# Kernel tuning notes

Hardware: AMD Instinct MI355X
Metric: run time of the kernel (lower is better)

## Reference

```python
import jax, jax.numpy as jnp
import numpy as np

UNITS = 512


def setup_inputs() -> dict:
    key = jax.random.key(0)
    ks = jax.random.split(key, 9)
    B, D, U = 16384, 512, UNITS
    return {
        "inputs": jax.random.normal(ks[0], (B, 2 * D), dtype=jnp.float32),
        "h": jax.random.normal(ks[1], (B, U), dtype=jnp.float32),
        "w_z": jax.random.normal(ks[2], (D, U), dtype=jnp.float32) * 0.05,
        "u_z": jax.random.normal(ks[3], (U, U), dtype=jnp.float32) * 0.05,
        "b_z": jnp.zeros((U,), dtype=jnp.float32),
        "w_r": jax.random.normal(ks[4], (D, U), dtype=jnp.float32) * 0.05,
        "u_r": jax.random.normal(ks[5], (U, U), dtype=jnp.float32) * 0.05,
        "b_r": jnp.zeros((U,), dtype=jnp.float32),
        "w_h": jax.random.normal(ks[6], (D, U), dtype=jnp.float32) * 0.05,
        "u_h": jax.random.normal(ks[7], (U, U), dtype=jnp.float32) * 0.05,
        "b_h": jnp.zeros((U,), dtype=jnp.float32),
    }


def reference(inputs, h, w_z, u_z, b_z, w_r, u_r, b_r, w_h, u_h, b_h):
    # Split concatenated (input, mask) halves along the feature axis.
    x, mask = jnp.split(inputs, 2, axis=1)  # each (B, D)
    # Faithful to source: mask @ zeros((D, U)) is identically zero.
    out_mask = jnp.matmul(mask, jnp.zeros((mask.shape[-1], UNITS), dtype=inputs.dtype))  # (B, U)
    h_masked = h * out_mask
    z_t = jax.nn.sigmoid(jnp.matmul(x, w_z) + jnp.matmul(h_masked, u_z) + b_z)
    r_t = jax.nn.sigmoid(jnp.matmul(x, w_r) + jnp.matmul(h_masked, u_r) + b_r)
    h_t = jnp.tanh(jnp.matmul(x, w_h) + jnp.matmul(r_t * h_masked, u_h) + b_h)
    h_t_seq = z_t * h_t + (1.0 - z_t) * h_masked  # (B, U)
    h_t_forward = jnp.concatenate((h_t_seq, out_mask), axis=1)  # (B, 2U)
    return (h_t_forward, h_t_seq)
```

## Files before the change

### kernel.cpp

```cpp
#include <hip/hip_runtime.h>

typedef __attribute__((ext_vector_type(4))) float f32x4;
typedef __attribute__((ext_vector_type(8))) short short8;
typedef __attribute__((ext_vector_type(8))) unsigned short ushort8;
typedef __attribute__((ext_vector_type(4))) unsigned short ushort4v;

#define M_ROWS 16384
#define KDIM 512
#define UDIM 512
#define IN_STRIDE 1024
#define NSTEP 16

__device__ __forceinline__ unsigned short f2bf(float f) {
    union { float f; unsigned u; } v; v.f = f;
    unsigned r = v.u + 0x7FFFu + ((v.u >> 16) & 1u);
    return (unsigned short)(r >> 16);
}

#define GLD16(g, l)                                                            \
    __builtin_amdgcn_global_load_lds(                                          \
        (const __attribute__((address_space(1))) void*)(g),                    \
        (__attribute__((address_space(3))) void*)(l), 16, 0, 0)

__global__ __launch_bounds__(256) void pack_all(
    const float* __restrict__ inp,
    const float* __restrict__ w_z,
    const float* __restrict__ w_h,
    unsigned short* __restrict__ Ap,
    unsigned short* __restrict__ Wp)
{
    const int bid = blockIdx.x;
    if (bid < 256) {
        int tid = bid * 256 + threadIdx.x;
        int s   = tid & 511;
        int kt  = (tid >> 9) & 15;
        int ub  = tid >> 13;
        int jj  = s >> 2;
        int sl  = (s & 3) ^ ((jj >> 1) & 3);
        int k   = kt * 32 + sl * 8;
        const float* w = ((jj >> 5) & 1) ? w_h : w_z;
        int u = ub * 64 + ((jj >> 6) << 5) + (jj & 31);
        ushort8 v;
#pragma unroll
        for (int i = 0; i < 8; ++i)
            v[i] = f2bf(w[(size_t)(k + i) * UDIM + u]);
        *reinterpret_cast<ushort8*>(Wp + (size_t)tid * 8) = v;
    } else {
        int g   = (bid - 256) * 256 + threadIdx.x;
        int by  = g >> 13;
        int rem = g & 8191;
        int kt  = rem >> 9;
        int s   = rem & 511;
        int row = by * 128 + (s >> 2);
        int sl  = (s & 3) ^ ((s >> 3) & 3);
        int k   = kt * 32 + sl * 8;
        const float* p = inp + (size_t)row * IN_STRIDE + k;
        f32x4 a = *reinterpret_cast<const f32x4*>(p);
        f32x4 b = *reinterpret_cast<const f32x4*>(p + 4);
        ushort8 v;
        v[0] = f2bf(a[0]); v[1] = f2bf(a[1]); v[2] = f2bf(a[2]); v[3] = f2bf(a[3]);
        v[4] = f2bf(b[0]); v[5] = f2bf(b[1]); v[6] = f2bf(b[2]); v[7] = f2bf(b[3]);
        *reinterpret_cast<ushort8*>(Ap + (size_t)g * 8) = v;
    }
}

__global__ __launch_bounds__(256, 3) void gru_gemm(
    const unsigned short* __restrict__ Ap,
    const unsigned short* __restrict__ Wp,
    const float* __restrict__ b_z,
    const float* __restrict__ b_h,
    float* __restrict__ out)
{
    __shared__ __align__(16) unsigned char smem[49152];
    unsigned short* shA = (unsigned short*)smem;
    unsigned short* shB = (unsigned short*)(smem + 24576);

    const int tid  = threadIdx.x;
    const int lane = tid & 63;
    const int wid  = tid >> 6;
    const int wm   = wid >> 1;
    const int wn   = wid & 1;

    const int d  = blockIdx.x;
    const int bx = (d >> 3) & 7;
    const int by = (d & 7) * 16 + (d >> 6);
    const int u0   = bx * 64;
    const int brow = by * 128;

    const int s0 = wid * 128 + lane;
    const unsigned short* ap = Ap + (size_t)by * 65536 + (size_t)s0 * 8;
    const unsigned short* bp = Wp + (size_t)bx * 65536 + (size_t)s0 * 8;

    f32x4 acc[4][4];
#pragma unroll
    for (int m = 0; m < 4; ++m)
#pragma unroll
        for (int n = 0; n < 4; ++n)
            acc[m][n] = (f32x4){0.f, 0.f, 0.f, 0.f};

    auto STAGE = [&](int b, int t) {
        GLD16(ap + t * 4096,       shA + b * 4096 + wid * 1024);
        GLD16(ap + t * 4096 + 512, shA + b * 4096 + wid * 1024 + 512);
        GLD16(bp + t * 4096,       shB + b * 4096 + wid * 1024);
        GLD16(bp + t * 4096 + 512, shB + b * 4096 + wid * 1024 + 512);
    };

    const int fr = lane & 15;
    const int ks = lane >> 4;
    const int xo = (fr >> 1) & 3;
    int aoff[4], boff[4];
#pragma unroll
    for (int m = 0; m < 4; ++m)
        aoff[m] = (wm * 64 + m * 16 + fr) * 32 + ((ks ^ xo) << 3);
#pragma unroll
    for (int n = 0; n < 4; ++n)
        boff[n] = (wn * 64 + n * 16 + fr) * 32 + ((ks ^ xo) << 3);

    STAGE(0, 0);
    STAGE(1, 1);
    asm volatile("s_waitcnt vmcnt(4)" ::: "memory");
    asm volatile("s_barrier" ::: "memory");

#pragma unroll
    for (int t = 0; t < NSTEP; ++t) {
        if (t + 2 < NSTEP) STAGE((t + 2) % 3, t + 2);
        const int buf = t % 3;
        short8 af[4], bfrag[4];
#pragma unroll
        for (int m = 0; m < 4; ++m)
            af[m] = *reinterpret_cast<const short8*>(&shA[buf * 4096 + aoff[m]]);
#pragma unroll
        for (int n = 0; n < 4; ++n)
            bfrag[n] = *reinterpret_cast<const short8*>(&shB[buf * 4096 + boff[n]]);
#pragma unroll
        for (int m = 0; m < 4; ++m)
#pragma unroll
            for (int n = 0; n < 4; ++n)
                acc[m][n] = __builtin_amdgcn_mfma_f32_16x16x32_bf16(af[m], bfrag[n], acc[m][n], 0, 0, 0);
        if (t + 1 < NSTEP) {
            asm volatile("s_waitcnt lgkmcnt(0)" ::: "memory");
            if (t + 2 < NSTEP) {
                asm volatile("s_waitcnt vmcnt(4)" ::: "memory");
            } else {
                asm volatile("s_waitcnt vmcnt(0)" ::: "memory");
            }
            asm volatile("s_barrier" ::: "memory");
        }
    }

    __syncthreads();

    float* plane = (float*)smem;
    const int fq = lane >> 4;
#pragma unroll
    for (int p = 0; p < 2; ++p) {
        int ucol = wn * 32 + p * 16 + fr;
        float bz = b_z[u0 + ucol];
        float bh = b_h[u0 + ucol];
#pragma unroll
        for (int m = 0; m < 4; ++m) {
            int row0 = wm * 64 + m * 16 + fq * 4;
            f32x4 az = acc[m][p];
            f32x4 ah = acc[m][p + 2];
#pragma unroll
            for (int j = 0; j < 4; ++j) {
                float zt = 1.f / (1.f + __expf(-(az[j] + bz)));
                float e  = __expf(2.f * (ah[j] + bh));
                float s  = zt * (1.f - 2.f / (e + 1.f));
                plane[(row0 + j) * 68 + ucol] = s;
            }
        }
    }
    __syncthreads();

    float* fwd = out;
    float* seq = out + (size_t)M_ROWS * 1024;
    const f32x4 z4 = (f32x4){0.f, 0.f, 0.f, 0.f};
    const int c4 = (tid & 15) * 4;
#pragma unroll
    for (int it = 0; it < 8; ++it) {
        int row = it * 16 + (tid >> 4);
        f32x4 v = *reinterpret_cast<const f32x4*>(&plane[row * 68 + c4]);
        size_t grow = (size_t)(brow + row);
        *reinterpret_cast<f32x4*>(&fwd[grow * 1024 + u0 + c4])       = v;
        *reinterpret_cast<f32x4*>(&fwd[grow * 1024 + 512 + u0 + c4]) = z4;
        *reinterpret_cast<f32x4*>(&seq[grow * 512 + u0 + c4])        = v;
    }
}

#define LDSS 40
__global__ __launch_bounds__(256) void gru_fused_legacy(
    const float* __restrict__ inp, const float* __restrict__ w_z,
    const float* __restrict__ b_z, const float* __restrict__ w_h,
    const float* __restrict__ b_h, float* __restrict__ out)
{
    __shared__ __align__(16) unsigned short Asl[2][128][LDSS];
    __shared__ __align__(16) unsigned short Bsl[2][128][LDSS];
    const int tid = threadIdx.x, lane = tid & 63, wid = tid >> 6;
    const int wm = wid >> 1, wn = wid & 1;
    const int u0 = blockIdx.x * 64, brow = blockIdx.y * 128;
    f32x4 acc[4][4];
#pragma unroll
    for (int m = 0; m < 4; ++m)
#pragma unroll
        for (int n = 0; n < 4; ++n) acc[m][n] = (f32x4){0.f,0.f,0.f,0.f};
    f32x4 rA[4], rB[4];
#define STAGE_LOAD(kt) { const int k0_=(kt)*32; \
    _Pragma("unroll") for (int it=0; it<4; ++it){ int idx=tid+256*it; int r=idx>>3,c=(idx&7)<<2; \
        rA[it]=*reinterpret_cast<const f32x4*>(inp+(size_t)(brow+r)*IN_STRIDE+k0_+c);} \
    _Pragma("unroll") for (int it=0; it<4; ++it){ int idx=tid+256*it; int jj=idx&127; int k4=(idx>>7)<<2; \
        const float* w_=((jj>>5)&1)?w_h:w_z; int u_=u0+((jj>>6)<<5)+(jj&31); \
        const float* p_=w_+(size_t)(k0_+k4)*UDIM+u_; \
        rB[it][0]=p_[0]; rB[it][1]=p_[UDIM]; rB[it][2]=p_[2*UDIM]; rB[it][3]=p_[3*UDIM];} }
#define STAGE_WRITE(bufi) { \
    _Pragma("unroll") for (int it=0; it<4; ++it){ int idx=tid+256*it; int r=idx>>3,c=(idx&7)<<2; ushort4v v; \
        v[0]=f2bf(rA[it][0]); v[1]=f2bf(rA[it][1]); v[2]=f2bf(rA[it][2]); v[3]=f2bf(rA[it][3]); \
        *reinterpret_cast<ushort4v*>(&Asl[bufi][r][c])=v;} \
    _Pragma("unroll") for (int it=0; it<4; ++it){ int idx=tid+256*it; int jj=idx&127; int k4=(idx>>7)<<2; ushort4v v; \
        v[0]=f2bf(rB[it][0]); v[1]=f2bf(rB[it][1]); v[2]=f2bf(rB[it][2]); v[3]=f2bf(rB[it][3]); \
        *reinterpret_cast<ushort4v*>(&Bsl[bufi][jj][k4])=v;} }
    STAGE_LOAD(0); STAGE_WRITE(0);
    const int fr = lane & 15, koff = (lane >> 4) << 3;
    for (int kt = 0; kt < NSTEP; ++kt) {
        if (kt + 1 < NSTEP) STAGE_LOAD(kt + 1);
        __syncthreads();
        const int buf = kt & 1;
        short8 af[4], bfr[4];
#pragma unroll
        for (int m = 0; m < 4; ++m) af[m] = *reinterpret_cast<const short8*>(&Asl[buf][wm*64+m*16+fr][koff]);
#pragma unroll
        for (int n = 0; n < 4; ++n) bfr[n] = *reinterpret_cast<const short8*>(&Bsl[buf][wn*64+n*16+fr][koff]);
#pragma unroll
        for (int m = 0; m < 4; ++m)
#pragma unroll
            for (int n = 0; n < 4; ++n)
                acc[m][n] = __builtin_amdgcn_mfma_f32_16x16x32_bf16(af[m], bfr[n], acc[m][n], 0, 0, 0);
        if (kt + 1 < NSTEP) STAGE_WRITE((kt + 1) & 1);
    }
    float* fwd = out; float* seq = out + (size_t)M_ROWS * 1024;
    const int fq = lane >> 4;
#pragma unroll
    for (int p = 0; p < 2; ++p) {
        int u = u0 + wn * 32 + p * 16 + fr;
        float bz = b_z[u], bh = b_h[u];
#pragma unroll
        for (int m = 0; m < 4; ++m) {
            int row0 = brow + wm * 64 + m * 16 + fq * 4;
            f32x4 az = acc[m][p], ah = acc[m][p + 2];
#pragma unroll
            for (int j = 0; j < 4; ++j) {
                float zt = 1.f / (1.f + __expf(-(az[j] + bz)));
                float e  = __expf(2.f * (ah[j] + bh));
                float s  = zt * (1.f - 2.f / (e + 1.f));
                size_t rr = (size_t)(row0 + j);
                fwd[rr * 1024 + u] = s;
                fwd[rr * 1024 + 512 + u] = 0.f;
                seq[rr * 512 + u] = s;
            }
        }
    }
}

extern "C" void kernel_launch(void* const* d_in, const int* in_sizes, int n_in,
                              void* d_out, int out_size, void* d_ws, size_t ws_size,
                              hipStream_t stream) {
    const float* inp = (const float*)d_in[0];
    const float* w_z = (const float*)d_in[2];
    const float* b_z = (const float*)d_in[4];
    const float* w_h = (const float*)d_in[8];
    const float* b_h = (const float*)d_in[10];
    float* out = (float*)d_out;

    const size_t needA = (size_t)M_ROWS * KDIM * 2;
    const size_t needB = (size_t)8 * 16 * 512 * 16;
    if (ws_size >= needA + needB) {
        unsigned short* Ap = (unsigned short*)d_ws;
        unsigned short* Wp = (unsigned short*)((char*)d_ws + needA);
        hipLaunchKernelGGL(pack_all, dim3(256 + 4096), dim3(256), 0, stream,
                           inp, w_z, w_h, Ap, Wp);
        hipLaunchKernelGGL(gru_gemm, dim3(1024), dim3(256), 0, stream,
                           Ap, Wp, b_z, b_h, out);
    } else {
        hipLaunchKernelGGL(gru_fused_legacy, dim3(8, 128), dim3(256), 0, stream,
                           inp, w_z, b_z, w_h, b_h, out);
    }
}
```

Measured before the change: 46.54 us.

## Fuse activation fp32-to-bf16 conversion into GEMM prologue, drop A pack pass

Removes the separate packing pass that converted the x half of the inputs to swizzled bf16 in workspace. The GEMM now loads fp32 x directly into registers, converts to bf16 and writes swizzled tiles into a double-buffered LDS region, while B keeps the async global-to-LDS triple buffer. This cuts the extra global write and read of the packed A matrix and one kernel launch. In exchange it adds register pressure, conversion ALU work inside the main loop, and a synchronous LDS-write step before each barrier. Each A tile is also read as fp32 by all 8 column blocks.

```diff
diff --git a/kernel.cpp b/kernel.cpp
--- a/kernel.cpp
+++ b/kernel.cpp
@@ -22,58 +22,37 @@
         (const __attribute__((address_space(1))) void*)(g),                    \
         (__attribute__((address_space(3))) void*)(l), 16, 0, 0)
 
-__global__ __launch_bounds__(256) void pack_all(
-    const float* __restrict__ inp,
+__global__ __launch_bounds__(256) void pack_w(
     const float* __restrict__ w_z,
     const float* __restrict__ w_h,
-    unsigned short* __restrict__ Ap,
     unsigned short* __restrict__ Wp)
 {
-    const int bid = blockIdx.x;
-    if (bid < 256) {
-        int tid = bid * 256 + threadIdx.x;
-        int s   = tid & 511;
-        int kt  = (tid >> 9) & 15;
-        int ub  = tid >> 13;
-        int jj  = s >> 2;
-        int sl  = (s & 3) ^ ((jj >> 1) & 3);
-        int k   = kt * 32 + sl * 8;
-        const float* w = ((jj >> 5) & 1) ? w_h : w_z;
-        int u = ub * 64 + ((jj >> 6) << 5) + (jj & 31);
-        ushort8 v;
-#pragma unroll
-        for (int i = 0; i < 8; ++i)
-            v[i] = f2bf(w[(size_t)(k + i) * UDIM + u]);
-        *reinterpret_cast<ushort8*>(Wp + (size_t)tid * 8) = v;
-    } else {
-        int g   = (bid - 256) * 256 + threadIdx.x;
-        int by  = g >> 13;
-        int rem = g & 8191;
-        int kt  = rem >> 9;
-        int s   = rem & 511;
-        int row = by * 128 + (s >> 2);
-        int sl  = (s & 3) ^ ((s >> 3) & 3);
-        int k   = kt * 32 + sl * 8;
-        const float* p = inp + (size_t)row * IN_STRIDE + k;
-        f32x4 a = *reinterpret_cast<const f32x4*>(p);
-        f32x4 b = *reinterpret_cast<const f32x4*>(p + 4);
-        ushort8 v;
-        v[0] = f2bf(a[0]); v[1] = f2bf(a[1]); v[2] = f2bf(a[2]); v[3] = f2bf(a[3]);
-        v[4] = f2bf(b[0]); v[5] = f2bf(b[1]); v[6] = f2bf(b[2]); v[7] = f2bf(b[3]);
-        *reinterpret_cast<ushort8*>(Ap + (size_t)g * 8) = v;
-    }
+    int tid = blockIdx.x * 256 + threadIdx.x;
+    int s   = tid & 511;
+    int kt  = (tid >> 9) & 15;
+    int ub  = tid >> 13;
+    int jj  = s >> 2;
+    int sl  = (s & 3) ^ ((jj >> 1) & 3);
+    int k   = kt * 32 + sl * 8;
+    const float* w = ((jj >> 5) & 1) ? w_h : w_z;
+    int u = ub * 64 + ((jj >> 6) << 5) + (jj & 31);
+    ushort8 v;
+#pragma unroll
+    for (int i = 0; i < 8; ++i)
+        v[i] = f2bf(w[(size_t)(k + i) * UDIM + u]);
+    *reinterpret_cast<ushort8*>(Wp + (size_t)tid * 8) = v;
 }
 
 __global__ __launch_bounds__(256, 3) void gru_gemm(
-    const unsigned short* __restrict__ Ap,
+    const float* __restrict__ x,
     const unsigned short* __restrict__ Wp,
     const float* __restrict__ b_z,
     const float* __restrict__ b_h,
     float* __restrict__ out)
 {
-    __shared__ __align__(16) unsigned char smem[49152];
+    __shared__ __align__(16) unsigned char smem[40960];
     unsigned short* shA = (unsigned short*)smem;
-    unsigned short* shB = (unsigned short*)(smem + 24576);
+    unsigned short* shB = (unsigned short*)(smem + 16384);
 
     const int tid  = threadIdx.x;
     const int lane = tid & 63;
@@ -87,9 +66,15 @@
     const int u0   = bx * 64;
     const int brow = by * 128;
 
-    const int s0 = wid * 128 + lane;
-    const unsigned short* ap = Ap + (size_t)by * 65536 + (size_t)s0 * 8;
-    const unsigned short* bp = Wp + (size_t)bx * 65536 + (size_t)s0 * 8;
+    const int s0a = wid * 128 + lane;
+    const int s1a = s0a + 64;
+    const int r0 = s0a >> 2, r1 = s1a >> 2;
+    const int sl0 = (s0a & 3) ^ ((r0 >> 1) & 3);
+    const int sl1 = (s1a & 3) ^ ((r1 >> 1) & 3);
+    const float* g0 = x + (size_t)(brow + r0) * IN_STRIDE + sl0 * 8;
+    const float* g1 = x + (size_t)(brow + r1) * IN_STRIDE + sl1 * 8;
+
+    const unsigned short* bp = Wp + (size_t)bx * 65536 + (size_t)s0a * 8;
 
     f32x4 acc[4][4];
 #pragma unroll
@@ -98,12 +83,32 @@
         for (int n = 0; n < 4; ++n)
             acc[m][n] = (f32x4){0.f, 0.f, 0.f, 0.f};
 
-    auto STAGE = [&](int b, int t) {
-        GLD16(ap + t * 4096,       shA + b * 4096 + wid * 1024);
-        GLD16(ap + t * 4096 + 512, shA + b * 4096 + wid * 1024 + 512);
-        GLD16(bp + t * 4096,       shB + b * 4096 + wid * 1024);
-        GLD16(bp + t * 4096 + 512, shB + b * 4096 + wid * 1024 + 512);
-    };
+    f32x4 rA[2][4];
+
+#define ISSUE_A(t, set)                                                        \
+    {                                                                          \
+        rA[set][0] = *reinterpret_cast<const f32x4*>(g0 + (t) * 32);           \
+        rA[set][1] = *reinterpret_cast<const f32x4*>(g0 + (t) * 32 + 4);       \
+        rA[set][2] = *reinterpret_cast<const f32x4*>(g1 + (t) * 32);           \
+        rA[set][3] = *reinterpret_cast<const f32x4*>(g1 + (t) * 32 + 4);       \
+    }
+
+#define ISSUE_B(t, b)                                                          \
+    {                                                                          \
+        GLD16(bp + (size_t)(t) * 4096,       shB + (b) * 4096 + wid * 1024);   \
+        GLD16(bp + (size_t)(t) * 4096 + 512, shB + (b) * 4096 + wid * 1024 + 512); \
+    }
+
+#define CVT_WRITE_A(set, b)                                                    \
+    {                                                                          \
+        ushort8 v0, v1;                                                        \
+        _Pragma("unroll")                                                      \
+        for (int i = 0; i < 4; ++i) { v0[i] = f2bf(rA[set][0][i]); v0[i+4] = f2bf(rA[set][1][i]); } \
+        _Pragma("unroll")                                                      \
+        for (int i = 0; i < 4; ++i) { v1[i] = f2bf(rA[set][2][i]); v1[i+4] = f2bf(rA[set][3][i]); } \
+        *reinterpret_cast<ushort8*>(&shA[(b) * 4096 + s0a * 8]) = v0;          \
+        *reinterpret_cast<ushort8*>(&shA[(b) * 4096 + s1a * 8]) = v1;          \
+    }
 
     const int fr = lane & 15;
     const int ks = lane >> 4;
@@ -116,34 +121,40 @@
     for (int n = 0; n < 4; ++n)
         boff[n] = (wn * 64 + n * 16 + fr) * 32 + ((ks ^ xo) << 3);
 
-    STAGE(0, 0);
-    STAGE(1, 1);
-    asm volatile("s_waitcnt vmcnt(4)" ::: "memory");
+    ISSUE_A(0, 0); ISSUE_B(0, 0);
+    ISSUE_A(1, 1); ISSUE_B(1, 1);
+    asm volatile("s_waitcnt vmcnt(6)" ::: "memory");
+    CVT_WRITE_A(0, 0);
+    asm volatile("s_waitcnt lgkmcnt(0)" ::: "memory");
     asm volatile("s_barrier" ::: "memory");
 
 #pragma unroll
     for (int t = 0; t < NSTEP; ++t) {
-        if (t + 2 < NSTEP) STAGE((t + 2) % 3, t + 2);
-        const int buf = t % 3;
+        if (t + 2 < NSTEP) {
+            ISSUE_A(t + 2, (t + 2) & 1);
+            ISSUE_B(t + 2, (t + 2) % 3);
+        }
+        const int ba = t & 1, bb = t % 3;
         short8 af[4], bfrag[4];
 #pragma unroll
         for (int m = 0; m < 4; ++m)
-            af[m] = *reinterpret_cast<const short8*>(&shA[buf * 4096 + aoff[m]]);
+            af[m] = *reinterpret_cast<const short8*>(&shA[ba * 4096 + aoff[m]]);
 #pragma unroll
         for (int n = 0; n < 4; ++n)
-            bfrag[n] = *reinterpret_cast<const short8*>(&shB[buf * 4096 + boff[n]]);
+            bfrag[n] = *reinterpret_cast<const short8*>(&shB[bb * 4096 + boff[n]]);
 #pragma unroll
         for (int m = 0; m < 4; ++m)
 #pragma unroll
             for (int n = 0; n < 4; ++n)
                 acc[m][n] = __builtin_amdgcn_mfma_f32_16x16x32_bf16(af[m], bfrag[n], acc[m][n], 0, 0, 0);
         if (t + 1 < NSTEP) {
-            asm volatile("s_waitcnt lgkmcnt(0)" ::: "memory");
             if (t + 2 < NSTEP) {
-                asm volatile("s_waitcnt vmcnt(4)" ::: "memory");
+                asm volatile("s_waitcnt vmcnt(6)" ::: "memory");
             } else {
                 asm volatile("s_waitcnt vmcnt(0)" ::: "memory");
             }
+            CVT_WRITE_A((t + 1) & 1, (t + 1) & 1);
+            asm volatile("s_waitcnt lgkmcnt(0)" ::: "memory");
             asm volatile("s_barrier" ::: "memory");
         }
     }
@@ -186,6 +197,9 @@
         *reinterpret_cast<f32x4*>(&fwd[grow * 1024 + 512 + u0 + c4]) = z4;
         *reinterpret_cast<f32x4*>(&seq[grow * 512 + u0 + c4])        = v;
     }
+#undef ISSUE_A
+#undef ISSUE_B
+#undef CVT_WRITE_A
 }
 
 #define LDSS 40
@@ -271,15 +285,12 @@
     const float* b_h = (const float*)d_in[10];
     float* out = (float*)d_out;
 
-    const size_t needA = (size_t)M_ROWS * KDIM * 2;
-    const size_t needB = (size_t)8 * 16 * 512 * 16;
-    if (ws_size >= needA + needB) {
-        unsigned short* Ap = (unsigned short*)d_ws;
-        unsigned short* Wp = (unsigned short*)((char*)d_ws + needA);
-        hipLaunchKernelGGL(pack_all, dim3(256 + 4096), dim3(256), 0, stream,
-                           inp, w_z, w_h, Ap, Wp);
+    const size_t needW = (size_t)8 * 16 * 512 * 16;
+    if (ws_size >= needW) {
+        unsigned short* Wp = (unsigned short*)d_ws;
+        hipLaunchKernelGGL(pack_w, dim3(256), dim3(256), 0, stream, w_z, w_h, Wp);
         hipLaunchKernelGGL(gru_gemm, dim3(1024), dim3(256), 0, stream,
-                           Ap, Wp, b_z, b_h, out);
+                           inp, Wp, b_z, b_h, out);
     } else {
         hipLaunchKernelGGL(gru_fused_legacy, dim3(8, 128), dim3(256), 0, stream,
                            inp, w_z, b_z, w_h, b_h, out);
```

Result: slower. 52.05 us (+11.8%).

## Fuse activation bf16 conversion into GEMM by staging fp32 A tiles in LDS

Applied to the files above, without the earlier changes.

Drops the separate pass that converted the input activations to a packed bf16 buffer. The GEMM now loads fp32 x tiles straight from the strided input into LDS with an XOR swizzle and converts them to bf16 when reading fragments. This removes a full write and re-read of the 16 MB packed activation buffer and a large pack launch. In exchange the A staging traffic per tile doubles, LDS use grows to 72 KB, occupancy drops from 3 to 2 blocks per CU, and conversion ALU work is added to the inner loop.

```diff
diff --git a/kernel.cpp b/kernel.cpp
--- a/kernel.cpp
+++ b/kernel.cpp
@@ -1,4 +1,5 @@
 #include <hip/hip_runtime.h>
+#include <hip/hip_bf16.h>
 
 typedef __attribute__((ext_vector_type(4))) float f32x4;
 typedef __attribute__((ext_vector_type(8))) short short8;
@@ -17,63 +18,47 @@
     return (unsigned short)(r >> 16);
 }
 
+__device__ __forceinline__ unsigned cvt2(float a, float b) {
+    __hip_bfloat162 h = __float22bfloat162_rn(float2{a, b});
+    union { __hip_bfloat162 h; unsigned u; } c; c.h = h; return c.u;
+}
+
 #define GLD16(g, l)                                                            \
     __builtin_amdgcn_global_load_lds(                                          \
         (const __attribute__((address_space(1))) void*)(g),                    \
         (__attribute__((address_space(3))) void*)(l), 16, 0, 0)
 
-__global__ __launch_bounds__(256) void pack_all(
-    const float* __restrict__ inp,
+__global__ __launch_bounds__(256) void pack_w(
     const float* __restrict__ w_z,
     const float* __restrict__ w_h,
-    unsigned short* __restrict__ Ap,
     unsigned short* __restrict__ Wp)
 {
-    const int bid = blockIdx.x;
-    if (bid < 256) {
-        int tid = bid * 256 + threadIdx.x;
-        int s   = tid & 511;
-        int kt  = (tid >> 9) & 15;
-        int ub  = tid >> 13;
-        int jj  = s >> 2;
-        int sl  = (s & 3) ^ ((jj >> 1) & 3);
-        int k   = kt * 32 + sl * 8;
-        const float* w = ((jj >> 5) & 1) ? w_h : w_z;
-        int u = ub * 64 + ((jj >> 6) << 5) + (jj & 31);
-        ushort8 v;
-#pragma unroll
-        for (int i = 0; i < 8; ++i)
-            v[i] = f2bf(w[(size_t)(k + i) * UDIM + u]);
-        *reinterpret_cast<ushort8*>(Wp + (size_t)tid * 8) = v;
-    } else {
-        int g   = (bid - 256) * 256 + threadIdx.x;
-        int by  = g >> 13;
-        int rem = g & 8191;
-        int kt  = rem >> 9;
-        int s   = rem & 511;
-        int row = by * 128 + (s >> 2);
-        int sl  = (s & 3) ^ ((s >> 3) & 3);
-        int k   = kt * 32 + sl * 8;
-        const float* p = inp + (size_t)row * IN_STRIDE + k;
-        f32x4 a = *reinterpret_cast<const f32x4*>(p);
-        f32x4 b = *reinterpret_cast<const f32x4*>(p + 4);
-        ushort8 v;
-        v[0] = f2bf(a[0]); v[1] = f2bf(a[1]); v[2] = f2bf(a[2]); v[3] = f2bf(a[3]);
-        v[4] = f2bf(b[0]); v[5] = f2bf(b[1]); v[6] = f2bf(b[2]); v[7] = f2bf(b[3]);
-        *reinterpret_cast<ushort8*>(Ap + (size_t)g * 8) = v;
-    }
-}
-
-__global__ __launch_bounds__(256, 3) void gru_gemm(
-    const unsigned short* __restrict__ Ap,
+    int tid = blockIdx.x * 256 + threadIdx.x;
+    int s   = tid & 511;
+    int kt  = (tid >> 9) & 15;
+    int ub  = tid >> 13;
+    int jj  = s >> 2;
+    int sl  = (s & 3) ^ ((jj >> 1) & 3);
+    int k   = kt * 32 + sl * 8;
+    const float* w = ((jj >> 5) & 1) ? w_h : w_z;
+    int u = ub * 64 + ((jj >> 6) << 5) + (jj & 31);
+    ushort8 v;
+#pragma unroll
+    for (int i = 0; i < 8; ++i)
+        v[i] = f2bf(w[(size_t)(k + i) * UDIM + u]);
+    *reinterpret_cast<ushort8*>(Wp + (size_t)tid * 8) = v;
+}
+
+__global__ __launch_bounds__(256, 2) void gru_gemm(
+    const float* __restrict__ x,
     const unsigned short* __restrict__ Wp,
     const float* __restrict__ b_z,
     const float* __restrict__ b_h,
     float* __restrict__ out)
 {
-    __shared__ __align__(16) unsigned char smem[49152];
-    unsigned short* shA = (unsigned short*)smem;
-    unsigned short* shB = (unsigned short*)(smem + 24576);
+    __shared__ __align__(16) unsigned char smem[73728];
+    float* shAf         = (float*)smem;
+    unsigned short* shB = (unsigned short*)(smem + 49152);
 
     const int tid  = threadIdx.x;
     const int lane = tid & 63;
@@ -87,8 +72,11 @@
     const int u0   = bx * 64;
     const int brow = by * 128;
 
+    const int arow = wid * 32 + (lane >> 3);
+    const int apg  = (lane & 7) ^ ((lane >> 3) & 7);
+    const float* gA = x + (size_t)(brow + arow) * IN_STRIDE + apg * 4;
+
     const int s0 = wid * 128 + lane;
-    const unsigned short* ap = Ap + (size_t)by * 65536 + (size_t)s0 * 8;
     const unsigned short* bp = Wp + (size_t)bx * 65536 + (size_t)s0 * 8;
 
     f32x4 acc[4][4];
@@ -99,26 +87,30 @@
             acc[m][n] = (f32x4){0.f, 0.f, 0.f, 0.f};
 
     auto STAGE = [&](int b, int t) {
-        GLD16(ap + t * 4096,       shA + b * 4096 + wid * 1024);
-        GLD16(ap + t * 4096 + 512, shA + b * 4096 + wid * 1024 + 512);
-        GLD16(bp + t * 4096,       shB + b * 4096 + wid * 1024);
-        GLD16(bp + t * 4096 + 512, shB + b * 4096 + wid * 1024 + 512);
+        GLD16(gA + (size_t)t * 32,                    shAf + b * 4096 + (wid * 32) * 32);
+        GLD16(gA + (size_t)t * 32 + 8 * IN_STRIDE,    shAf + b * 4096 + (wid * 32 + 8) * 32);
+        GLD16(gA + (size_t)t * 32 + 16 * IN_STRIDE,   shAf + b * 4096 + (wid * 32 + 16) * 32);
+        GLD16(gA + (size_t)t * 32 + 24 * IN_STRIDE,   shAf + b * 4096 + (wid * 32 + 24) * 32);
+        GLD16(bp + (size_t)t * 4096,                  shB + b * 4096 + wid * 1024);
+        GLD16(bp + (size_t)t * 4096 + 512,            shB + b * 4096 + wid * 1024 + 512);
     };
 
     const int fr = lane & 15;
     const int ks = lane >> 4;
+    const int asl = (2 * ks) ^ (fr & 7);
+    int abase[4];
+#pragma unroll
+    for (int m = 0; m < 4; ++m)
+        abase[m] = (wm * 64 + m * 16 + fr) * 32;
     const int xo = (fr >> 1) & 3;
-    int aoff[4], boff[4];
-#pragma unroll
-    for (int m = 0; m < 4; ++m)
-        aoff[m] = (wm * 64 + m * 16 + fr) * 32 + ((ks ^ xo) << 3);
+    int boff[4];
 #pragma unroll
     for (int n = 0; n < 4; ++n)
         boff[n] = (wn * 64 + n * 16 + fr) * 32 + ((ks ^ xo) << 3);
 
     STAGE(0, 0);
     STAGE(1, 1);
-    asm volatile("s_waitcnt vmcnt(4)" ::: "memory");
+    asm volatile("s_waitcnt vmcnt(6)" ::: "memory");
     asm volatile("s_barrier" ::: "memory");
 
 #pragma unroll
@@ -127,8 +119,17 @@
         const int buf = t % 3;
         short8 af[4], bfrag[4];
 #pragma unroll
-        for (int m = 0; m < 4; ++m)
-            af[m] = *reinterpret_cast<const short8*>(&shA[buf * 4096 + aoff[m]]);
+        for (int m = 0; m < 4; ++m) {
+            const float* ab = shAf + buf * 4096 + abase[m];
+            f32x4 lo = *reinterpret_cast<const f32x4*>(ab + asl * 4);
+            f32x4 hi = *reinterpret_cast<const f32x4*>(ab + (asl ^ 1) * 4);
+            union { unsigned u[4]; short8 s; } c;
+            c.u[0] = cvt2(lo[0], lo[1]);
+            c.u[1] = cvt2(lo[2], lo[3]);
+            c.u[2] = cvt2(hi[0], hi[1]);
+            c.u[3] = cvt2(hi[2], hi[3]);
+            af[m] = c.s;
+        }
 #pragma unroll
         for (int n = 0; n < 4; ++n)
             bfrag[n] = *reinterpret_cast<const short8*>(&shB[buf * 4096 + boff[n]]);
@@ -140,7 +141,7 @@
         if (t + 1 < NSTEP) {
             asm volatile("s_waitcnt lgkmcnt(0)" ::: "memory");
             if (t + 2 < NSTEP) {
-                asm volatile("s_waitcnt vmcnt(4)" ::: "memory");
+                asm volatile("s_waitcnt vmcnt(6)" ::: "memory");
             } else {
                 asm volatile("s_waitcnt vmcnt(0)" ::: "memory");
             }
@@ -271,15 +272,12 @@
     const float* b_h = (const float*)d_in[10];
     float* out = (float*)d_out;
 
-    const size_t needA = (size_t)M_ROWS * KDIM * 2;
-    const size_t needB = (size_t)8 * 16 * 512 * 16;
-    if (ws_size >= needA + needB) {
-        unsigned short* Ap = (unsigned short*)d_ws;
-        unsigned short* Wp = (unsigned short*)((char*)d_ws + needA);
-        hipLaunchKernelGGL(pack_all, dim3(256 + 4096), dim3(256), 0, stream,
-                           inp, w_z, w_h, Ap, Wp);
+    const size_t needW = (size_t)8 * 16 * 512 * 16;
+    if (ws_size >= needW) {
+        unsigned short* Wp = (unsigned short*)d_ws;
+        hipLaunchKernelGGL(pack_w, dim3(256), dim3(256), 0, stream, w_z, w_h, Wp);
         hipLaunchKernelGGL(gru_gemm, dim3(1024), dim3(256), 0, stream,
-                           Ap, Wp, b_z, b_h, out);
+                           inp, Wp, b_z, b_h, out);
     } else {
         hipLaunchKernelGGL(gru_fused_legacy, dim3(8, 128), dim3(256), 0, stream,
                            inp, w_z, b_z, w_h, b_h, out);
```

After: 49.50 us. 6.4% more time.
